# Kernel optimization log

Measured on AMD Instinct MI355X. Metric: run time of the kernel, lower is better.

The kernel has to match this reference:

```python
import jax, jax.numpy as jnp
import numpy as np

EPS = 1e-05


def setup_inputs() -> dict:
    key = jax.random.key(0)
    B, T, C = 8, 8192, 512
    x = jax.random.normal(key, (B, T, C), dtype=jnp.float32)
    # Learned per-channel scale; module initializes it to ones.
    weight = jnp.ones((C,), dtype=jnp.float32)
    return {"x": x, "weight": weight}


def reference(x, weight):
    """Cumulative (running) group norm over the frame axis.

    x: [B, T, C]; stats are accumulated over channels AND all frames <= t.
    """
    input_dtype = x.dtype
    xc = x.astype(jnp.float32)
    B, T, C = xc.shape

    # Per-frame channel sum, then cumulative sum over time -> [B, T, 1]
    cum_sum = jnp.cumsum(jnp.sum(xc, axis=-1, keepdims=True), axis=1)
    # Element count up to frame t: (t+1) * C (mask is all-ones here)
    cum_count = (jnp.arange(1, T + 1, dtype=jnp.float32) * C).reshape(1, T, 1)
    cum_count = jnp.maximum(cum_count, 1.0)

    cum_mean = cum_sum / cum_count  # [B, T, 1]

    # Squared deviation from the *running* mean, summed over channels, cumsum over time.
    sq_diff = jnp.square(xc - cum_mean)  # [B, T, C]
    cum_var = jnp.cumsum(jnp.sum(sq_diff, axis=-1, keepdims=True), axis=1) / cum_count

    normalized = (xc - cum_mean) * jax.lax.rsqrt(cum_var + EPS)
    out = normalized * weight.astype(jnp.float32)  # broadcast over [B, T, C]
    return out.astype(input_dtype)
```

## Files before the change

### kernel.cpp

```cpp
#include <hip/hip_runtime.h>

#define EPS 1e-5f

__global__ __launch_bounds__(256) void frame_stats_kernel(
    const float* __restrict__ x, float* __restrict__ s_arr,
    float* __restrict__ q_arr, int nframes) {
  int wave = threadIdx.x >> 6;
  int lane = threadIdx.x & 63;
  int frame = blockIdx.x * 4 + wave;
  if (frame >= nframes) return;
  const float4* xb = (const float4*)(x + (size_t)frame * 512);
  float4 a = xb[lane];
  float4 b = xb[64 + lane];
  float s = a.x + a.y + a.z + a.w + b.x + b.y + b.z + b.w;
  float q = a.x * a.x + a.y * a.y + a.z * a.z + a.w * a.w +
            b.x * b.x + b.y * b.y + b.z * b.z + b.w * b.w;
#pragma unroll
  for (int off = 32; off >= 1; off >>= 1) {
    s += __shfl_down(s, off);
    q += __shfl_down(q, off);
  }
  if (lane == 0) {
    s_arr[frame] = s;
    q_arr[frame] = q;
  }
}

__global__ __launch_bounds__(64) void scan_kernel(
    const float* __restrict__ s_arr, const float* __restrict__ q_arr,
    float* __restrict__ mean_arr, float* __restrict__ inv_arr, int T) {
  int b = blockIdx.x;
  int lane = threadIdx.x;
  const float4* s4p = (const float4*)(s_arr + (size_t)b * T);
  const float4* q4p = (const float4*)(q_arr + (size_t)b * T);
  float4* m4p = (float4*)(mean_arr + (size_t)b * T);
  float4* i4p = (float4*)(inv_arr + (size_t)b * T);
  float carryS = 0.f, carryV = 0.f;
  int niter = T >> 8;
  for (int it = 0; it < niter; ++it) {
    int idx4 = (it << 6) + lane;
    float4 s4 = s4p[idx4];
    float4 q4 = q4p[idx4];

    float p0 = s4.x;
    float p1 = p0 + s4.y;
    float p2 = p1 + s4.z;
    float p3 = p2 + s4.w;
    float tot = p3;
    float incl = tot;
#pragma unroll
    for (int off = 1; off < 64; off <<= 1) {
      float n = __shfl_up(incl, off);
      if (lane >= off) incl += n;
    }
    float excl = incl - tot;
    float base = carryS + excl;
    carryS += __shfl(incl, 63);

    int t0 = (it << 8) + (lane << 2);
    float c0 = (float)(t0 + 1) * 512.f;
    float c1 = (float)(t0 + 2) * 512.f;
    float c2 = (float)(t0 + 3) * 512.f;
    float c3 = (float)(t0 + 4) * 512.f;
    float m0 = (base + p0) / c0;
    float m1 = (base + p1) / c1;
    float m2 = (base + p2) / c2;
    float m3 = (base + p3) / c3;

    float v0 = q4.x - 2.f * m0 * s4.x + 512.f * m0 * m0;
    float v1 = q4.y - 2.f * m1 * s4.y + 512.f * m1 * m1;
    float v2 = q4.z - 2.f * m2 * s4.z + 512.f * m2 * m2;
    float v3 = q4.w - 2.f * m3 * s4.w + 512.f * m3 * m3;

    float r0 = v0;
    float r1 = r0 + v1;
    float r2 = r1 + v2;
    float r3 = r2 + v3;
    float totv = r3;
    float inclv = totv;
#pragma unroll
    for (int off = 1; off < 64; off <<= 1) {
      float n = __shfl_up(inclv, off);
      if (lane >= off) inclv += n;
    }
    float exclv = inclv - totv;
    float basev = carryV + exclv;
    carryV += __shfl(inclv, 63);

    float4 mo, io;
    mo.x = m0; mo.y = m1; mo.z = m2; mo.w = m3;
    io.x = rsqrtf((basev + r0) / c0 + EPS);
    io.y = rsqrtf((basev + r1) / c1 + EPS);
    io.z = rsqrtf((basev + r2) / c2 + EPS);
    io.w = rsqrtf((basev + r3) / c3 + EPS);
    m4p[idx4] = mo;
    i4p[idx4] = io;
  }
}

__global__ __launch_bounds__(256) void apply_kernel(
    const float* __restrict__ x, const float* __restrict__ weight,
    const float* __restrict__ mean_arr, const float* __restrict__ inv_arr,
    float* __restrict__ out, long n4) {
  long i = (long)blockIdx.x * blockDim.x + threadIdx.x;
  if (i >= n4) return;
  int frame = (int)(i >> 7);
  int c4 = (int)(i & 127);
  float4 xv = ((const float4*)x)[i];
  float4 wv = ((const float4*)weight)[c4];
  float m = mean_arr[frame];
  float inv = inv_arr[frame];
  float4 o;
  o.x = (xv.x - m) * inv * wv.x;
  o.y = (xv.y - m) * inv * wv.y;
  o.z = (xv.z - m) * inv * wv.z;
  o.w = (xv.w - m) * inv * wv.w;
  ((float4*)out)[i] = o;
}

extern "C" void kernel_launch(void* const* d_in, const int* in_sizes, int n_in,
                              void* d_out, int out_size, void* d_ws,
                              size_t ws_size, hipStream_t stream) {
  const float* x = (const float*)d_in[0];
  const float* w = (const float*)d_in[1];
  float* out = (float*)d_out;
  const int B = 8, T = 8192;
  const int BT = B * T;

  float* s_arr = (float*)d_ws;
  float* q_arr = s_arr + BT;
  float* mean_arr = q_arr + BT;
  float* inv_arr = mean_arr + BT;

  frame_stats_kernel<<<BT / 4, 256, 0, stream>>>(x, s_arr, q_arr, BT);
  scan_kernel<<<B, 64, 0, stream>>>(s_arr, q_arr, mean_arr, inv_arr, T);
  long n4 = (long)BT * 128;
  apply_kernel<<<(int)((n4 + 255) / 256), 256, 0, stream>>>(
      x, w, mean_arr, inv_arr, out, n4);
}
```

Baseline: 273.4 us.

## Fuse stats, scan and apply into one cooperative kernel with grid syncs

Replaces the three separate launches (frame stats, per-batch scan, elementwise apply) with a single cooperative kernel of 1024 blocks that uses grid.sync between phases. Each block handles 64 frames, so the second read of x in the apply phase can hit in the large on-chip cache (the input is 128MB, MI355X has 256MB Infinity Cache). The scan now uses 256 threads per batch with an LDS cross-wave combine, and outputs are written with nontemporal stores. Risks include grid-sync overhead, the scan phase idling all but 8 blocks, and the cooperative launch needing every block resident at once.

```diff
diff --git a/kernel.cpp b/kernel.cpp
--- a/kernel.cpp
+++ b/kernel.cpp
@@ -1,121 +1,162 @@
 #include <hip/hip_runtime.h>
+#include <hip/hip_cooperative_groups.h>
+
+namespace cg = cooperative_groups;
 
 #define EPS 1e-5f
 
-__global__ __launch_bounds__(256) void frame_stats_kernel(
-    const float* __restrict__ x, float* __restrict__ s_arr,
-    float* __restrict__ q_arr, int nframes) {
-  int wave = threadIdx.x >> 6;
-  int lane = threadIdx.x & 63;
-  int frame = blockIdx.x * 4 + wave;
-  if (frame >= nframes) return;
-  const float4* xb = (const float4*)(x + (size_t)frame * 512);
-  float4 a = xb[lane];
-  float4 b = xb[64 + lane];
-  float s = a.x + a.y + a.z + a.w + b.x + b.y + b.z + b.w;
-  float q = a.x * a.x + a.y * a.y + a.z * a.z + a.w * a.w +
-            b.x * b.x + b.y * b.y + b.z * b.z + b.w * b.w;
+typedef float nfloat4 __attribute__((ext_vector_type(4)));
+
+__global__ __launch_bounds__(256, 4) void cgn_fused(
+    const float* __restrict__ x, const float* __restrict__ w,
+    float* __restrict__ out, float* __restrict__ ws) {
+  const int T = 8192;
+  const int BT = 8 * T;
+  float* s_arr = ws;
+  float* q_arr = ws + BT;
+  float* mean_arr = ws + 2 * BT;
+  float* inv_arr = ws + 3 * BT;
+
+  __shared__ float lds_s[4];
+  __shared__ float lds_v[4];
+
+  cg::grid_group grid = cg::this_grid();
+  const int tid = threadIdx.x;
+  const int lane = tid & 63;
+  const int wid = tid >> 6;
+
+  const int f0 = blockIdx.x * 64 + wid * 16;
+  const nfloat4* x4 = (const nfloat4*)x;
+#pragma unroll 4
+  for (int f = 0; f < 16; ++f) {
+    const int frame = f0 + f;
+    const nfloat4* fb = x4 + (size_t)frame * 128;
+    nfloat4 a = fb[lane];
+    nfloat4 b = fb[64 + lane];
+    float s = a.x + a.y + a.z + a.w + b.x + b.y + b.z + b.w;
+    float q = a.x * a.x + a.y * a.y + a.z * a.z + a.w * a.w +
+              b.x * b.x + b.y * b.y + b.z * b.z + b.w * b.w;
 #pragma unroll
-  for (int off = 32; off >= 1; off >>= 1) {
-    s += __shfl_down(s, off);
-    q += __shfl_down(q, off);
+    for (int off = 32; off >= 1; off >>= 1) {
+      s += __shfl_down(s, off);
+      q += __shfl_down(q, off);
+    }
+    if (lane == 0) {
+      s_arr[frame] = s;
+      q_arr[frame] = q;
+    }
   }
-  if (lane == 0) {
-    s_arr[frame] = s;
-    q_arr[frame] = q;
+
+  grid.sync();
+
+  if (blockIdx.x < 8) {
+    const int b = blockIdx.x;
+    const nfloat4* s4p = (const nfloat4*)(s_arr + (size_t)b * T);
+    const nfloat4* q4p = (const nfloat4*)(q_arr + (size_t)b * T);
+    nfloat4* m4p = (nfloat4*)(mean_arr + (size_t)b * T);
+    nfloat4* i4p = (nfloat4*)(inv_arr + (size_t)b * T);
+    float carryS = 0.f, carryV = 0.f;
+#pragma unroll 1
+    for (int c = 0; c < 8; ++c) {
+      const int idx4 = (c << 8) + tid;
+      nfloat4 s4 = s4p[idx4];
+      nfloat4 q4 = q4p[idx4];
+
+      float p0 = s4.x;
+      float p1 = p0 + s4.y;
+      float p2 = p1 + s4.z;
+      float p3 = p2 + s4.w;
+      float tot = p3, incl = tot;
+#pragma unroll
+      for (int off = 1; off < 64; off <<= 1) {
+        float n = __shfl_up(incl, off);
+        if (lane >= off) incl += n;
+      }
+      if (lane == 63) lds_s[wid] = incl;
+      __syncthreads();
+      float waveExclS = 0.f, chunkTotS = 0.f;
+#pragma unroll
+      for (int wv = 0; wv < 4; ++wv) {
+        float tv = lds_s[wv];
+        if (wv < wid) waveExclS += tv;
+        chunkTotS += tv;
+      }
+      float base = carryS + waveExclS + (incl - tot);
+      carryS += chunkTotS;
+
+      const int t0 = (c << 10) + (tid << 2);
+      float c0 = (float)(t0 + 1) * 512.f;
+      float c1 = (float)(t0 + 2) * 512.f;
+      float c2 = (float)(t0 + 3) * 512.f;
+      float c3 = (float)(t0 + 4) * 512.f;
+      float m0 = (base + p0) / c0;
+      float m1 = (base + p1) / c1;
+      float m2 = (base + p2) / c2;
+      float m3 = (base + p3) / c3;
+
+      float v0 = q4.x - 2.f * m0 * s4.x + 512.f * m0 * m0;
+      float v1 = q4.y - 2.f * m1 * s4.y + 512.f * m1 * m1;
+      float v2 = q4.z - 2.f * m2 * s4.z + 512.f * m2 * m2;
+      float v3 = q4.w - 2.f * m3 * s4.w + 512.f * m3 * m3;
+
+      float r0 = v0;
+      float r1 = r0 + v1;
+      float r2 = r1 + v2;
+      float r3 = r2 + v3;
+      float totv = r3, inclv = totv;
+#pragma unroll
+      for (int off = 1; off < 64; off <<= 1) {
+        float n = __shfl_up(inclv, off);
+        if (lane >= off) inclv += n;
+      }
+      if (lane == 63) lds_v[wid] = inclv;
+      __syncthreads();
+      float waveExclV = 0.f, chunkTotV = 0.f;
+#pragma unroll
+      for (int wv = 0; wv < 4; ++wv) {
+        float tv = lds_v[wv];
+        if (wv < wid) waveExclV += tv;
+        chunkTotV += tv;
+      }
+      float baseV = carryV + waveExclV + (inclv - totv);
+      carryV += chunkTotV;
+
+      nfloat4 mo, io;
+      mo.x = m0; mo.y = m1; mo.z = m2; mo.w = m3;
+      io.x = rsqrtf((baseV + r0) / c0 + EPS);
+      io.y = rsqrtf((baseV + r1) / c1 + EPS);
+      io.z = rsqrtf((baseV + r2) / c2 + EPS);
+      io.w = rsqrtf((baseV + r3) / c3 + EPS);
+      m4p[idx4] = mo;
+      i4p[idx4] = io;
+    }
   }
-}
 
-__global__ __launch_bounds__(64) void scan_kernel(
-    const float* __restrict__ s_arr, const float* __restrict__ q_arr,
-    float* __restrict__ mean_arr, float* __restrict__ inv_arr, int T) {
-  int b = blockIdx.x;
-  int lane = threadIdx.x;
-  const float4* s4p = (const float4*)(s_arr + (size_t)b * T);
-  const float4* q4p = (const float4*)(q_arr + (size_t)b * T);
-  float4* m4p = (float4*)(mean_arr + (size_t)b * T);
-  float4* i4p = (float4*)(inv_arr + (size_t)b * T);
-  float carryS = 0.f, carryV = 0.f;
-  int niter = T >> 8;
-  for (int it = 0; it < niter; ++it) {
-    int idx4 = (it << 6) + lane;
-    float4 s4 = s4p[idx4];
-    float4 q4 = q4p[idx4];
+  grid.sync();
 
-    float p0 = s4.x;
-    float p1 = p0 + s4.y;
-    float p2 = p1 + s4.z;
-    float p3 = p2 + s4.w;
-    float tot = p3;
-    float incl = tot;
-#pragma unroll
-    for (int off = 1; off < 64; off <<= 1) {
-      float n = __shfl_up(incl, off);
-      if (lane >= off) incl += n;
-    }
-    float excl = incl - tot;
-    float base = carryS + excl;
-    carryS += __shfl(incl, 63);
-
-    int t0 = (it << 8) + (lane << 2);
-    float c0 = (float)(t0 + 1) * 512.f;
-    float c1 = (float)(t0 + 2) * 512.f;
-    float c2 = (float)(t0 + 3) * 512.f;
-    float c3 = (float)(t0 + 4) * 512.f;
-    float m0 = (base + p0) / c0;
-    float m1 = (base + p1) / c1;
-    float m2 = (base + p2) / c2;
-    float m3 = (base + p3) / c3;
-
-    float v0 = q4.x - 2.f * m0 * s4.x + 512.f * m0 * m0;
-    float v1 = q4.y - 2.f * m1 * s4.y + 512.f * m1 * m1;
-    float v2 = q4.z - 2.f * m2 * s4.z + 512.f * m2 * m2;
-    float v3 = q4.w - 2.f * m3 * s4.w + 512.f * m3 * m3;
-
-    float r0 = v0;
-    float r1 = r0 + v1;
-    float r2 = r1 + v2;
-    float r3 = r2 + v3;
-    float totv = r3;
-    float inclv = totv;
-#pragma unroll
-    for (int off = 1; off < 64; off <<= 1) {
-      float n = __shfl_up(inclv, off);
-      if (lane >= off) inclv += n;
-    }
-    float exclv = inclv - totv;
-    float basev = carryV + exclv;
-    carryV += __shfl(inclv, 63);
-
-    float4 mo, io;
-    mo.x = m0; mo.y = m1; mo.z = m2; mo.w = m3;
-    io.x = rsqrtf((basev + r0) / c0 + EPS);
-    io.y = rsqrtf((basev + r1) / c1 + EPS);
-    io.z = rsqrtf((basev + r2) / c2 + EPS);
-    io.w = rsqrtf((basev + r3) / c3 + EPS);
-    m4p[idx4] = mo;
-    i4p[idx4] = io;
+  const nfloat4 wa = ((const nfloat4*)w)[lane];
+  const nfloat4 wb = ((const nfloat4*)w)[64 + lane];
+  nfloat4* out4 = (nfloat4*)out;
+#pragma unroll 4
+  for (int f = 0; f < 16; ++f) {
+    const int frame = f0 + f;
+    const float m = mean_arr[frame];
+    const float iv = inv_arr[frame];
+    const nfloat4* fb = x4 + (size_t)frame * 128;
+    nfloat4 a = fb[lane];
+    nfloat4 b = fb[64 + lane];
+    nfloat4 oa, ob;
+    oa.x = (a.x - m) * iv * wa.x;
+    oa.y = (a.y - m) * iv * wa.y;
+    oa.z = (a.z - m) * iv * wa.z;
+    oa.w = (a.w - m) * iv * wa.w;
+    ob.x = (b.x - m) * iv * wb.x;
+    ob.y = (b.y - m) * iv * wb.y;
+    ob.z = (b.z - m) * iv * wb.z;
+    ob.w = (b.w - m) * iv * wb.w;
+    __builtin_nontemporal_store(oa, out4 + (size_t)frame * 128 + lane);
+    __builtin_nontemporal_store(ob, out4 + (size_t)frame * 128 + 64 + lane);
   }
-}
-
-__global__ __launch_bounds__(256) void apply_kernel(
-    const float* __restrict__ x, const float* __restrict__ weight,
-    const float* __restrict__ mean_arr, const float* __restrict__ inv_arr,
-    float* __restrict__ out, long n4) {
-  long i = (long)blockIdx.x * blockDim.x + threadIdx.x;
-  if (i >= n4) return;
-  int frame = (int)(i >> 7);
-  int c4 = (int)(i & 127);
-  float4 xv = ((const float4*)x)[i];
-  float4 wv = ((const float4*)weight)[c4];
-  float m = mean_arr[frame];
-  float inv = inv_arr[frame];
-  float4 o;
-  o.x = (xv.x - m) * inv * wv.x;
-  o.y = (xv.y - m) * inv * wv.y;
-  o.z = (xv.z - m) * inv * wv.z;
-  o.w = (xv.w - m) * inv * wv.w;
-  ((float4*)out)[i] = o;
 }
 
 extern "C" void kernel_launch(void* const* d_in, const int* in_sizes, int n_in,
@@ -124,17 +165,9 @@
   const float* x = (const float*)d_in[0];
   const float* w = (const float*)d_in[1];
   float* out = (float*)d_out;
-  const int B = 8, T = 8192;
-  const int BT = B * T;
+  float* ws = (float*)d_ws;
 
-  float* s_arr = (float*)d_ws;
-  float* q_arr = s_arr + BT;
-  float* mean_arr = q_arr + BT;
-  float* inv_arr = mean_arr + BT;
-
-  frame_stats_kernel<<<BT / 4, 256, 0, stream>>>(x, s_arr, q_arr, BT);
-  scan_kernel<<<B, 64, 0, stream>>>(s_arr, q_arr, mean_arr, inv_arr, T);
-  long n4 = (long)BT * 128;
-  apply_kernel<<<(int)((n4 + 255) / 256), 256, 0, stream>>>(
-      x, w, mean_arr, inv_arr, out, n4);
+  void* kargs[] = {(void*)&x, (void*)&w, (void*)&out, (void*)&ws};
+  (void)hipLaunchCooperativeKernel((const void*)cgn_fused, dim3(1024),
+                                   dim3(256), kargs, 0, stream);
 }
```

After: 461.7 us. +68.9%, slower.

## Parallelize per-batch scan across 1024 threads and use nontemporal output stores

Applied to the files above, without the earlier changes.

The scan kernel used to walk each batch's 8192 frames serially in 32 iterations with a single wave. It now uses 1024 threads per batch, each handling 8 frames, and combines wave totals through LDS. This removes the serial latency chain in the middle kernel, at the cost of two block barriers and a different summation order for the carries. The apply kernel also drops its bounds checks and writes the output with nontemporal stores to reduce cache pollution.

```diff
diff --git a/kernel.cpp b/kernel.cpp
--- a/kernel.cpp
+++ b/kernel.cpp
@@ -2,16 +2,18 @@
 
 #define EPS 1e-5f
 
+typedef float nfloat4 __attribute__((ext_vector_type(4)));
+
+
 __global__ __launch_bounds__(256) void frame_stats_kernel(
     const float* __restrict__ x, float* __restrict__ s_arr,
-    float* __restrict__ q_arr, int nframes) {
-  int wave = threadIdx.x >> 6;
-  int lane = threadIdx.x & 63;
-  int frame = blockIdx.x * 4 + wave;
-  if (frame >= nframes) return;
-  const float4* xb = (const float4*)(x + (size_t)frame * 512);
-  float4 a = xb[lane];
-  float4 b = xb[64 + lane];
+    float* __restrict__ q_arr) {
+  const int wave = threadIdx.x >> 6;
+  const int lane = threadIdx.x & 63;
+  const int frame = blockIdx.x * 4 + wave;
+  const nfloat4* xb = (const nfloat4*)(x + (size_t)frame * 512);
+  nfloat4 a = xb[lane];
+  nfloat4 b = xb[64 + lane];
   float s = a.x + a.y + a.z + a.w + b.x + b.y + b.z + b.w;
   float q = a.x * a.x + a.y * a.y + a.z * a.z + a.w * a.w +
             b.x * b.x + b.y * b.y + b.z * b.z + b.w * b.w;
@@ -26,96 +28,133 @@
   }
 }
 
-__global__ __launch_bounds__(64) void scan_kernel(
+__global__ __launch_bounds__(1024) void scan_kernel(
     const float* __restrict__ s_arr, const float* __restrict__ q_arr,
-    float* __restrict__ mean_arr, float* __restrict__ inv_arr, int T) {
-  int b = blockIdx.x;
-  int lane = threadIdx.x;
-  const float4* s4p = (const float4*)(s_arr + (size_t)b * T);
-  const float4* q4p = (const float4*)(q_arr + (size_t)b * T);
-  float4* m4p = (float4*)(mean_arr + (size_t)b * T);
-  float4* i4p = (float4*)(inv_arr + (size_t)b * T);
-  float carryS = 0.f, carryV = 0.f;
-  int niter = T >> 8;
-  for (int it = 0; it < niter; ++it) {
-    int idx4 = (it << 6) + lane;
-    float4 s4 = s4p[idx4];
-    float4 q4 = q4p[idx4];
+    float* __restrict__ mean_arr, float* __restrict__ inv_arr) {
+  const int T = 8192;
+  const int b = blockIdx.x;
+  const int tid = threadIdx.x;
+  const int lane = tid & 63;
+  const int wid = tid >> 6;
 
-    float p0 = s4.x;
-    float p1 = p0 + s4.y;
-    float p2 = p1 + s4.z;
-    float p3 = p2 + s4.w;
-    float tot = p3;
-    float incl = tot;
+  __shared__ float lds_s[16];
+  __shared__ float lds_v[16];
+
+  const nfloat4* s4p = (const nfloat4*)(s_arr + (size_t)b * T);
+  const nfloat4* q4p = (const nfloat4*)(q_arr + (size_t)b * T);
+  nfloat4* m4p = (nfloat4*)(mean_arr + (size_t)b * T);
+  nfloat4* i4p = (nfloat4*)(inv_arr + (size_t)b * T);
+
+  nfloat4 sa = s4p[2 * tid];
+  nfloat4 sb = s4p[2 * tid + 1];
+  nfloat4 qa = q4p[2 * tid];
+  nfloat4 qb = q4p[2 * tid + 1];
+
+  float p0 = sa.x;
+  float p1 = p0 + sa.y;
+  float p2 = p1 + sa.z;
+  float p3 = p2 + sa.w;
+  float p4 = p3 + sb.x;
+  float p5 = p4 + sb.y;
+  float p6 = p5 + sb.z;
+  float p7 = p6 + sb.w;
+  float tot = p7, incl = tot;
 #pragma unroll
-    for (int off = 1; off < 64; off <<= 1) {
-      float n = __shfl_up(incl, off);
-      if (lane >= off) incl += n;
-    }
-    float excl = incl - tot;
-    float base = carryS + excl;
-    carryS += __shfl(incl, 63);
+  for (int off = 1; off < 64; off <<= 1) {
+    float n = __shfl_up(incl, off);
+    if (lane >= off) incl += n;
+  }
+  if (lane == 63) lds_s[wid] = incl;
+  __syncthreads();
+  float waveExcl = 0.f;
+#pragma unroll
+  for (int wv = 0; wv < 16; ++wv)
+    if (wv < wid) waveExcl += lds_s[wv];
+  float base = waveExcl + incl - tot;
 
-    int t0 = (it << 8) + (lane << 2);
-    float c0 = (float)(t0 + 1) * 512.f;
-    float c1 = (float)(t0 + 2) * 512.f;
-    float c2 = (float)(t0 + 3) * 512.f;
-    float c3 = (float)(t0 + 4) * 512.f;
-    float m0 = (base + p0) / c0;
-    float m1 = (base + p1) / c1;
-    float m2 = (base + p2) / c2;
-    float m3 = (base + p3) / c3;
+  const int t0 = tid << 3;
+  float c0 = (float)(t0 + 1) * 512.f;
+  float c1 = (float)(t0 + 2) * 512.f;
+  float c2 = (float)(t0 + 3) * 512.f;
+  float c3 = (float)(t0 + 4) * 512.f;
+  float c4 = (float)(t0 + 5) * 512.f;
+  float c5 = (float)(t0 + 6) * 512.f;
+  float c6 = (float)(t0 + 7) * 512.f;
+  float c7 = (float)(t0 + 8) * 512.f;
+  float m0 = (base + p0) / c0;
+  float m1 = (base + p1) / c1;
+  float m2 = (base + p2) / c2;
+  float m3 = (base + p3) / c3;
+  float m4 = (base + p4) / c4;
+  float m5 = (base + p5) / c5;
+  float m6 = (base + p6) / c6;
+  float m7 = (base + p7) / c7;
 
-    float v0 = q4.x - 2.f * m0 * s4.x + 512.f * m0 * m0;
-    float v1 = q4.y - 2.f * m1 * s4.y + 512.f * m1 * m1;
-    float v2 = q4.z - 2.f * m2 * s4.z + 512.f * m2 * m2;
-    float v3 = q4.w - 2.f * m3 * s4.w + 512.f * m3 * m3;
+  float v0 = qa.x - 2.f * m0 * sa.x + 512.f * m0 * m0;
+  float v1 = qa.y - 2.f * m1 * sa.y + 512.f * m1 * m1;
+  float v2 = qa.z - 2.f * m2 * sa.z + 512.f * m2 * m2;
+  float v3 = qa.w - 2.f * m3 * sa.w + 512.f * m3 * m3;
+  float v4 = qb.x - 2.f * m4 * sb.x + 512.f * m4 * m4;
+  float v5 = qb.y - 2.f * m5 * sb.y + 512.f * m5 * m5;
+  float v6 = qb.z - 2.f * m6 * sb.z + 512.f * m6 * m6;
+  float v7 = qb.w - 2.f * m7 * sb.w + 512.f * m7 * m7;
 
-    float r0 = v0;
-    float r1 = r0 + v1;
-    float r2 = r1 + v2;
-    float r3 = r2 + v3;
-    float totv = r3;
-    float inclv = totv;
+  float r0 = v0;
+  float r1 = r0 + v1;
+  float r2 = r1 + v2;
+  float r3 = r2 + v3;
+  float r4 = r3 + v4;
+  float r5 = r4 + v5;
+  float r6 = r5 + v6;
+  float r7 = r6 + v7;
+  float totv = r7, inclv = totv;
 #pragma unroll
-    for (int off = 1; off < 64; off <<= 1) {
-      float n = __shfl_up(inclv, off);
-      if (lane >= off) inclv += n;
-    }
-    float exclv = inclv - totv;
-    float basev = carryV + exclv;
-    carryV += __shfl(inclv, 63);
+  for (int off = 1; off < 64; off <<= 1) {
+    float n = __shfl_up(inclv, off);
+    if (lane >= off) inclv += n;
+  }
+  if (lane == 63) lds_v[wid] = inclv;
+  __syncthreads();
+  float waveExclV = 0.f;
+#pragma unroll
+  for (int wv = 0; wv < 16; ++wv)
+    if (wv < wid) waveExclV += lds_v[wv];
+  float baseV = waveExclV + inclv - totv;
 
-    float4 mo, io;
-    mo.x = m0; mo.y = m1; mo.z = m2; mo.w = m3;
-    io.x = rsqrtf((basev + r0) / c0 + EPS);
-    io.y = rsqrtf((basev + r1) / c1 + EPS);
-    io.z = rsqrtf((basev + r2) / c2 + EPS);
-    io.w = rsqrtf((basev + r3) / c3 + EPS);
-    m4p[idx4] = mo;
-    i4p[idx4] = io;
-  }
+  nfloat4 moa, mob, ioa, iob;
+  moa.x = m0; moa.y = m1; moa.z = m2; moa.w = m3;
+  mob.x = m4; mob.y = m5; mob.z = m6; mob.w = m7;
+  ioa.x = rsqrtf((baseV + r0) / c0 + EPS);
+  ioa.y = rsqrtf((baseV + r1) / c1 + EPS);
+  ioa.z = rsqrtf((baseV + r2) / c2 + EPS);
+  ioa.w = rsqrtf((baseV + r3) / c3 + EPS);
+  iob.x = rsqrtf((baseV + r4) / c4 + EPS);
+  iob.y = rsqrtf((baseV + r5) / c5 + EPS);
+  iob.z = rsqrtf((baseV + r6) / c6 + EPS);
+  iob.w = rsqrtf((baseV + r7) / c7 + EPS);
+  m4p[2 * tid] = moa;
+  m4p[2 * tid + 1] = mob;
+  i4p[2 * tid] = ioa;
+  i4p[2 * tid + 1] = iob;
 }
 
 __global__ __launch_bounds__(256) void apply_kernel(
     const float* __restrict__ x, const float* __restrict__ weight,
     const float* __restrict__ mean_arr, const float* __restrict__ inv_arr,
-    float* __restrict__ out, long n4) {
-  long i = (long)blockIdx.x * blockDim.x + threadIdx.x;
-  if (i >= n4) return;
-  int frame = (int)(i >> 7);
-  int c4 = (int)(i & 127);
-  float4 xv = ((const float4*)x)[i];
-  float4 wv = ((const float4*)weight)[c4];
+    float* __restrict__ out) {
+  const long i = (long)blockIdx.x * blockDim.x + threadIdx.x;
+  const int frame = (int)(i >> 7);
+  const int c4 = (int)(i & 127);
+  nfloat4 xv = ((const nfloat4*)x)[i];
+  nfloat4 wv = ((const nfloat4*)weight)[c4];
   float m = mean_arr[frame];
   float inv = inv_arr[frame];
-  float4 o;
+  nfloat4 o;
   o.x = (xv.x - m) * inv * wv.x;
   o.y = (xv.y - m) * inv * wv.y;
   o.z = (xv.z - m) * inv * wv.z;
   o.w = (xv.w - m) * inv * wv.w;
-  ((float4*)out)[i] = o;
+  __builtin_nontemporal_store(o, (nfloat4*)out + i);
 }
 
 extern "C" void kernel_launch(void* const* d_in, const int* in_sizes, int n_in,
@@ -132,9 +171,9 @@
   float* mean_arr = q_arr + BT;
   float* inv_arr = mean_arr + BT;
 
-  frame_stats_kernel<<<BT / 4, 256, 0, stream>>>(x, s_arr, q_arr, BT);
-  scan_kernel<<<B, 64, 0, stream>>>(s_arr, q_arr, mean_arr, inv_arr, T);
-  long n4 = (long)BT * 128;
-  apply_kernel<<<(int)((n4 + 255) / 256), 256, 0, stream>>>(
-      x, w, mean_arr, inv_arr, out, n4);
+  frame_stats_kernel<<<BT / 4, 256, 0, stream>>>(x, s_arr, q_arr);
+  scan_kernel<<<B, 1024, 0, stream>>>(s_arr, q_arr, mean_arr, inv_arr);
+  const long n4 = (long)BT * 128;
+  apply_kernel<<<(int)(n4 / 256), 256, 0, stream>>>(x, w, mean_arr, inv_arr,
+                                                    out);
 }
```

Result: faster. 248.1 us (-9.2%).
